# Kernel optimization log

Measured on AMD Instinct MI355X. Metric: run time of the kernel, lower is better.

Reference implementation:

```python
import jax, jax.numpy as jnp
import numpy as np

NFEAT = 128
NHID = 64
NLAYER = 3
N_NODES = 50000
N_EDGES = 800000
N_GRAPHS = 512
BN_EPS = 1e-5


def _bn(x, gamma, beta):
    # BatchNorm1d in training mode: biased batch stats over the node axis.
    m = x.mean(axis=0)
    v = x.var(axis=0)
    return (x - m) * jax.lax.rsqrt(v + BN_EPS) * gamma + beta


def _pool(x, batch):
    # global_mean_pool: segment mean over graph ids.
    s = jax.ops.segment_sum(x, batch, num_segments=N_GRAPHS)
    c = jax.ops.segment_sum(jnp.ones((x.shape[0], 1), x.dtype), batch, num_segments=N_GRAPHS)
    return s / jnp.maximum(c, 1.0)


def setup_inputs() -> dict:
    key = jax.random.key(0)
    ks = jax.random.split(key, 16)
    x = jax.random.normal(ks[0], (N_NODES, NFEAT), dtype=jnp.float32)
    edge_index = jax.random.randint(ks[1], (2, N_EDGES), 0, N_NODES, dtype=jnp.int64)
    batch = jnp.sort(jax.random.randint(ks[2], (N_NODES,), 0, N_GRAPHS, dtype=jnp.int64))
    s_in = 1.0 / np.sqrt(NFEAT)
    s_h = 1.0 / np.sqrt(NHID)
    return {
        "x": x,
        "edge_index": edge_index,
        "batch": batch,
        "Wt": jax.random.uniform(ks[3], (NFEAT, NHID), jnp.float32, -s_in, s_in),
        "bt": jax.random.uniform(ks[4], (NHID,), jnp.float32, -s_in, s_in),
        "gt": jnp.ones((NHID,), jnp.float32),
        "bet": jnp.zeros((NHID,), jnp.float32),
        "W1": jax.random.uniform(ks[5], (NLAYER, NHID, NHID), jnp.float32, -s_h, s_h),
        "b1": jax.random.uniform(ks[6], (NLAYER, NHID), jnp.float32, -s_h, s_h),
        "W2": jax.random.uniform(ks[7], (NLAYER, NHID, NHID), jnp.float32, -s_h, s_h),
        "b2": jax.random.uniform(ks[8], (NLAYER, NHID), jnp.float32, -s_h, s_h),
        "g": jnp.ones((NLAYER, NHID), jnp.float32),
        "be": jnp.zeros((NLAYER, NHID), jnp.float32),
    }


def reference(x, edge_index, batch, Wt, bt, gt, bet, W1, b1, W2, b2, g, be):
    n = x.shape[0]
    src, dst = edge_index[0], edge_index[1]
    # input transform: Linear + BN
    h = _bn(x @ Wt + bt, gt, bet)
    embeds = [_pool(h, batch)]
    for l in range(NLAYER):
        # GINConv, eps=0: mlp(x_i + sum_{j->i} x_j); flow source->target
        agg = jax.ops.segment_sum(h[src], dst, num_segments=n)
        z = h + agg
        z = jax.nn.relu(z @ W1[l] + b1[l]) @ W2[l] + b2[l]
        h = jax.nn.relu(_bn(z, g[l], be[l]))
        embeds.append(_pool(h, batch))
    return jnp.stack(embeds)  # [NLAYER+1, N_GRAPHS, NHID]
```

## Files before the change

### kernel.cpp

```cpp
#include <hip/hip_runtime.h>

#define NFEAT   128
#define NHID    64
#define NLAYER  3
#define NNODES  50000
#define NEDGES  800000
#define NGRAPHS 512
#define BN_EPS  1e-5f
#define MLPB    1563
#define CAP     64
#define PADW    68

typedef unsigned short u16;
typedef __attribute__((ext_vector_type(8))) short bf8;
typedef __attribute__((ext_vector_type(4))) float f32x4;

__device__ inline float b2f(u16 v) { return __uint_as_float(((unsigned)v) << 16); }
__device__ inline u16 f2b(float f) {
    unsigned u = __float_as_uint(f);
    return (u16)((u + 0x7FFF + ((u >> 16) & 1)) >> 16);
}
__device__ inline bf8 ldb8(const u16* p) {
    union { uint2 a[2]; bf8 v; } u;
    u.a[0] = *(const uint2*)p;
    u.a[1] = *(const uint2*)(p + 4);
    return u.v;
}
__device__ inline bf8 ldb8g(const u16* p) {
    union { uint4 a; bf8 v; } u;
    u.a = *(const uint4*)p;
    return u.v;
}
__device__ inline void add8(float* a, const uint4 v) {
    a[0] += __uint_as_float(v.x << 16);
    a[1] += __uint_as_float(v.x & 0xFFFF0000u);
    a[2] += __uint_as_float(v.y << 16);
    a[3] += __uint_as_float(v.y & 0xFFFF0000u);
    a[4] += __uint_as_float(v.z << 16);
    a[5] += __uint_as_float(v.z & 0xFFFF0000u);
    a[6] += __uint_as_float(v.w << 16);
    a[7] += __uint_as_float(v.w & 0xFFFF0000u);
}
__device__ inline void unp8(float* a, const uint4 v) {
    a[0] = __uint_as_float(v.x << 16);
    a[1] = __uint_as_float(v.x & 0xFFFF0000u);
    a[2] = __uint_as_float(v.y << 16);
    a[3] = __uint_as_float(v.y & 0xFFFF0000u);
    a[4] = __uint_as_float(v.z << 16);
    a[5] = __uint_as_float(v.z & 0xFFFF0000u);
    a[6] = __uint_as_float(v.w << 16);
    a[7] = __uint_as_float(v.w & 0xFFFF0000u);
}
__device__ inline uint2 pack4(float a, float b, float c, float d) {
    uint2 r;
    r.x = (unsigned)f2b(a) | ((unsigned)f2b(b) << 16);
    r.y = (unsigned)f2b(c) | ((unsigned)f2b(d) << 16);
    return r;
}

__global__ __launch_bounds__(256) void k_fill(const int* __restrict__ ei,
                                              int* __restrict__ deg,
                                              int* __restrict__ col) {
    int rangeId = blockIdx.x & 7, chunk = blockIdx.x >> 3;
    int lo = rangeId * (NNODES / 8), hi = lo + (NNODES / 8);
    int ebeg = chunk * (NEDGES / 256), eend = ebeg + (NEDGES / 256);
    for (int e = ebeg + threadIdx.x; e < eend; e += 256) {
        int dst = ei[NEDGES + e];
        if (dst >= lo && dst < hi) {
            int slot = atomicAdd(&deg[dst], 1);
            if (slot < CAP) col[dst * CAP + slot] = ei[e];
        }
    }
}

__global__ __launch_bounds__(256) void k_goff(const int* __restrict__ batch,
                                              int* __restrict__ gstart) {
    int gph = blockIdx.x * 256 + threadIdx.x;
    if (gph > NGRAPHS) return;
    if (gph == NGRAPHS) { gstart[NGRAPHS] = NNODES; return; }
    int lo = 0, hi = NNODES;
    while (lo < hi) {
        int mid = (lo + hi) >> 1;
        if (batch[mid] < gph) lo = mid + 1; else hi = mid;
    }
    gstart[gph] = lo;
}

__global__ __launch_bounds__(256) void k_wcvt(const float* __restrict__ Wt,
                                              const float* __restrict__ W1,
                                              const float* __restrict__ W2,
                                              u16* __restrict__ wtin,
                                              u16* __restrict__ wt) {
    int idx = blockIdx.x * 256 + threadIdx.x;
    if (idx < NFEAT * NHID) {
        int n = idx >> 7, k = idx & 127;
        wtin[n * NFEAT + k] = f2b(Wt[k * NHID + n]);
        return;
    }
    idx -= NFEAT * NHID;
    if (idx < NLAYER * NHID * NHID) {
        int l = idx >> 12, rem = idx & 4095, n = rem >> 6, k = rem & 63;
        wt[l * 8192 + n * 64 + k]        = f2b(W1[l * 4096 + k * 64 + n]);
        wt[l * 8192 + 4096 + n * 64 + k] = f2b(W2[l * 4096 + k * 64 + n]);
    }
}

__global__ __launch_bounds__(256) void k_gemm_in(const float* __restrict__ x,
                                                 const u16* __restrict__ wtin,
                                                 const float* __restrict__ bt,
                                                 u16* __restrict__ zout,
                                                 float* __restrict__ partials) {
    __shared__ u16 sx[32][132];
    __shared__ float ps[128];
    int tid = threadIdx.x;
    int base = blockIdx.x * 32;
#pragma unroll
    for (int i = 0; i < 4; ++i) {
        int idx = i * 256 + tid;
        int row = idx >> 5, kq = idx & 31;
        int rc = min(base + row, NNODES - 1);
        float4 v = ((const float4*)(x + (long long)rc * NFEAT))[kq];
        *(uint2*)&sx[row][kq * 4] = pack4(v.x, v.y, v.z, v.w);
    }
    __syncthreads();
    int w = tid >> 6, lane = tid & 63;
    int m = lane & 15, g = lane >> 4;
    int ncol = w * 16 + m;
    bool hiv = (base + 16 < NNODES);
    float bb = bt[ncol];
    f32x4 cl = {bb, bb, bb, bb}, ch = {bb, bb, bb, bb};
    const u16* wn = wtin + ncol * NFEAT;
#pragma unroll
    for (int s = 0; s < 4; ++s) {
        int k0 = s * 32 + g * 8;
        bf8 B  = ldb8g(wn + k0);
        bf8 Al = ldb8(&sx[m][k0]);
        bf8 Ah = ldb8(&sx[16 + m][k0]);
        cl = __builtin_amdgcn_mfma_f32_16x16x32_bf16(Al, B, cl, 0, 0, 0);
        ch = __builtin_amdgcn_mfma_f32_16x16x32_bf16(Ah, B, ch, 0, 0, 0);
    }
    float s1 = cl[0] + cl[1] + cl[2] + cl[3];
    float s2 = cl[0] * cl[0] + cl[1] * cl[1] + cl[2] * cl[2] + cl[3] * cl[3];
    if (hiv) {
        s1 += ch[0] + ch[1] + ch[2] + ch[3];
        s2 += ch[0] * ch[0] + ch[1] * ch[1] + ch[2] * ch[2] + ch[3] * ch[3];
    }
    s1 += __shfl_xor(s1, 16, 64); s1 += __shfl_xor(s1, 32, 64);
    s2 += __shfl_xor(s2, 16, 64); s2 += __shfl_xor(s2, 32, 64);
    if (lane < 16) {
        ps[w * 16 + lane] = s1;
        ps[64 + w * 16 + lane] = s2;
    }
#pragma unroll
    for (int i = 0; i < 4; ++i) {
        zout[(base + g * 4 + i) * NHID + ncol] = f2b(cl[i]);
        if (hiv) zout[(base + 16 + g * 4 + i) * NHID + ncol] = f2b(ch[i]);
    }
    __syncthreads();
    if (tid < 128) partials[blockIdx.x * 128 + tid] = ps[tid];
}

__global__ __launch_bounds__(256) void k_red(const float* __restrict__ partials,
                                             float* __restrict__ stats, int np) {
    __shared__ float red[4];
    int c = blockIdx.x, t = threadIdx.x;
    float s = 0.f;
    for (int i = t; i < np; i += 256) s += partials[i * 128 + c];
#pragma unroll
    for (int off = 32; off >= 1; off >>= 1) s += __shfl_xor(s, off, 64);
    if ((t & 63) == 0) red[t >> 6] = s;
    __syncthreads();
    if (t == 0) stats[c] = red[0] + red[1] + red[2] + red[3];
}

__global__ __launch_bounds__(256) void k_bnh(const u16* __restrict__ z,
                                             const float* __restrict__ stats,
                                             const float* __restrict__ gamma,
                                             const float* __restrict__ beta,
                                             u16* __restrict__ h) {
    int idx = blockIdx.x * 256 + threadIdx.x;
    if (idx >= NNODES * NHID / 8) return;
    int j0 = (idx & 7) * 8;
    uint4 v = ((const uint4*)z)[idx];
    float o[8];
    unp8(o, v);
#pragma unroll
    for (int k = 0; k < 8; ++k) {
        int j = j0 + k;
        float m = stats[j] * (1.0f / NNODES);
        float var = stats[64 + j] * (1.0f / NNODES) - m * m;
        float sc = rsqrtf(var + BN_EPS) * gamma[j];
        o[k] = fmaxf(fmaf(o[k], sc, beta[j] - m * sc), 0.f);
    }
    uint4 w;
    uint2 p0 = pack4(o[0], o[1], o[2], o[3]);
    uint2 p1 = pack4(o[4], o[5], o[6], o[7]);
    w.x = p0.x; w.y = p0.y; w.z = p1.x; w.w = p1.y;
    ((uint4*)h)[idx] = w;
}

__global__ __launch_bounds__(256) void k_pool(const u16* __restrict__ z,
                                              const float* __restrict__ stats,
                                              const float* __restrict__ gamma,
                                              const float* __restrict__ beta,
                                              const int* __restrict__ gstart,
                                              float* __restrict__ out) {
    __shared__ float4 red[4][16];
    int gph = blockIdx.x;
    int lane = threadIdx.x & 63, w = threadIdx.x >> 6;
    int c = lane & 15, ws = lane >> 4;
    int slot = w * 4 + ws;
    int j0 = c * 4;
    float sc[4], sh[4];
#pragma unroll
    for (int k = 0; k < 4; ++k) {
        int j = j0 + k;
        float m = stats[j] * (1.0f / NNODES);
        float var = stats[64 + j] * (1.0f / NNODES) - m * m;
        sc[k] = rsqrtf(var + BN_EPS) * gamma[j];
        sh[k] = beta[j] - m * sc[k];
    }
    const ushort4* z4 = (const ushort4*)z;
    int s0 = gstart[gph], e0 = gstart[gph + 1];
    float a[4] = {0.f, 0.f, 0.f, 0.f};
    for (int r = s0 + slot; r < e0; r += 16) {
        ushort4 v = z4[r * 16 + c];
        a[0] += fmaxf(fmaf(b2f(v.x), sc[0], sh[0]), 0.f);
        a[1] += fmaxf(fmaf(b2f(v.y), sc[1], sh[1]), 0.f);
        a[2] += fmaxf(fmaf(b2f(v.z), sc[2], sh[2]), 0.f);
        a[3] += fmaxf(fmaf(b2f(v.w), sc[3], sh[3]), 0.f);
    }
#pragma unroll
    for (int k = 0; k < 4; ++k) {
        a[k] += __shfl_xor(a[k], 16, 64);
        a[k] += __shfl_xor(a[k], 32, 64);
    }
    if (lane < 16) red[w][c] = make_float4(a[0], a[1], a[2], a[3]);
    __syncthreads();
    if (threadIdx.x < 16) {
        float4 r0 = red[0][threadIdx.x], r1 = red[1][threadIdx.x];
        float4 r2 = red[2][threadIdx.x], r3 = red[3][threadIdx.x];
        float inv = 1.0f / fmaxf((float)(e0 - s0), 1.0f);
        float* o = &out[gph * NHID + threadIdx.x * 4];
        o[0] = (r0.x + r1.x + r2.x + r3.x) * inv;
        o[1] = (r0.y + r1.y + r2.y + r3.y) * inv;
        o[2] = (r0.z + r1.z + r2.z + r3.z) * inv;
        o[3] = (r0.w + r1.w + r2.w + r3.w) * inv;
    }
}

template <int AFFINE>
__global__ __launch_bounds__(256) void k_mlp(const u16* __restrict__ hin,
                                             const float* __restrict__ stats,
                                             const float* __restrict__ gamma,
                                             const float* __restrict__ beta,
                                             const int* __restrict__ batch,
                                             const int* __restrict__ deg,
                                             const int* __restrict__ col,
                                             const u16* __restrict__ w1t,
                                             const float* __restrict__ b1,
                                             const u16* __restrict__ w2t,
                                             const float* __restrict__ b2,
                                             u16* __restrict__ zout,
                                             float* __restrict__ partials,
                                             float* __restrict__ poolacc) {
    __shared__ u16 szb[32][PADW];
    __shared__ u16 stb[32][PADW];
    __shared__ float ps[128];
    int tid = threadIdx.x;
    int w = tid >> 6, lane = tid & 63;
    int nd = lane >> 3, c8 = lane & 7;
    int node = w * 8 + nd;
    int base = blockIdx.x * 32;
    int r = base + node;
    bool rv = (r < NNODES);
    int rc = rv ? r : (NNODES - 1);
    const uint4* h16 = (const uint4*)hin;

    float sc[8], sh[8];
    if (AFFINE) {
#pragma unroll
        for (int k = 0; k < 8; ++k) {
            int j = c8 * 8 + k;
            float m = stats[j] * (1.0f / NNODES);
            float var = stats[64 + j] * (1.0f / NNODES) - m * m;
            sc[k] = rsqrtf(var + BN_EPS) * gamma[j];
            sh[k] = beta[j] - m * sc[k];
        }
    }

    float acc[8], acc2[8] = {0, 0, 0, 0, 0, 0, 0, 0};
    float selfh[8];
    {
        uint4 sv = h16[rc * 8 + c8];
        unp8(acc, sv);
#pragma unroll
        for (int k = 0; k < 8; ++k)
            selfh[k] = AFFINE ? fmaf(acc[k], sc[k], sh[k]) : acc[k];
    }
    int dd = rv ? min(deg[r], CAP) : 0;
    {
        const int* cp = col + rc * CAP;
        int t = 0;
        for (; t + 8 <= dd; t += 8) {
            int4 ia = *(const int4*)(cp + t);
            int4 ib = *(const int4*)(cp + t + 4);
            uint4 v0 = h16[ia.x * 8 + c8];
            uint4 v1 = h16[ia.y * 8 + c8];
            uint4 v2 = h16[ia.z * 8 + c8];
            uint4 v3 = h16[ia.w * 8 + c8];
            uint4 v4 = h16[ib.x * 8 + c8];
            uint4 v5 = h16[ib.y * 8 + c8];
            uint4 v6 = h16[ib.z * 8 + c8];
            uint4 v7 = h16[ib.w * 8 + c8];
            add8(acc, v0); add8(acc2, v1); add8(acc, v2); add8(acc2, v3);
            add8(acc, v4); add8(acc2, v5); add8(acc, v6); add8(acc2, v7);
        }
        if (t + 4 <= dd) {
            int4 ia = *(const int4*)(cp + t);
            uint4 v0 = h16[ia.x * 8 + c8];
            uint4 v1 = h16[ia.y * 8 + c8];
            uint4 v2 = h16[ia.z * 8 + c8];
            uint4 v3 = h16[ia.w * 8 + c8];
            add8(acc, v0); add8(acc2, v1); add8(acc, v2); add8(acc2, v3);
            t += 4;
        }
        for (; t < dd; ++t) {
            uint4 v0 = h16[cp[t] * 8 + c8];
            add8(acc, v0);
        }
    }
    {
        float zv[8];
#pragma unroll
        for (int k = 0; k < 8; ++k) {
            float s = acc[k] + acc2[k];
            zv[k] = AFFINE ? fmaf(s, sc[k], (float)(1 + dd) * sh[k]) : s;
            if (!rv) zv[k] = 0.f;
        }
        *(uint2*)&szb[node][c8 * 8]     = pack4(zv[0], zv[1], zv[2], zv[3]);
        *(uint2*)&szb[node][c8 * 8 + 4] = pack4(zv[4], zv[5], zv[6], zv[7]);
    }

    {
        int r0 = base + w * 8;
        int myg = rv ? batch[r] : -1;
        int g_lo = batch[min(r0, NNODES - 1)];
        int g_hi = batch[min(r0 + 7, NNODES - 1)];
        for (int gg = g_lo; gg <= g_hi; ++gg) {
            float v[8];
#pragma unroll
            for (int k = 0; k < 8; ++k) {
                v[k] = (myg == gg) ? selfh[k] : 0.f;
                v[k] += __shfl_xor(v[k], 8, 64);
                v[k] += __shfl_xor(v[k], 16, 64);
                v[k] += __shfl_xor(v[k], 32, 64);
            }
            if (lane < 8) {
                float* p = &poolacc[gg * NHID + lane * 8];
#pragma unroll
                for (int k = 0; k < 8; ++k) atomicAdd(p + k, v[k]);
            }
        }
    }
    __syncthreads();

    int m = lane & 15, g = lane >> 4;
    int ncol = w * 16 + m;
    bool hiv = (base + 16 < NNODES);
    const u16* w1n = w1t + ncol * 64;
    const u16* w2n = w2t + ncol * 64;

    bf8 Al0 = ldb8(&szb[m][g * 8]);
    bf8 Al1 = ldb8(&szb[m][32 + g * 8]);
    bf8 Ah0 = ldb8(&szb[16 + m][g * 8]);
    bf8 Ah1 = ldb8(&szb[16 + m][32 + g * 8]);
    bf8 B0 = ldb8g(w1n + g * 8);
    bf8 B1 = ldb8g(w1n + 32 + g * 8);
    float bb1 = b1[ncol];
    f32x4 cl = {bb1, bb1, bb1, bb1}, ch = {bb1, bb1, bb1, bb1};
    cl = __builtin_amdgcn_mfma_f32_16x16x32_bf16(Al0, B0, cl, 0, 0, 0);
    cl = __builtin_amdgcn_mfma_f32_16x16x32_bf16(Al1, B1, cl, 0, 0, 0);
    ch = __builtin_amdgcn_mfma_f32_16x16x32_bf16(Ah0, B0, ch, 0, 0, 0);
    ch = __builtin_amdgcn_mfma_f32_16x16x32_bf16(Ah1, B1, ch, 0, 0, 0);
#pragma unroll
    for (int i = 0; i < 4; ++i) {
        stb[g * 4 + i][ncol]      = f2b(fmaxf(cl[i], 0.f));
        stb[16 + g * 4 + i][ncol] = f2b(fmaxf(ch[i], 0.f));
    }
    __syncthreads();

    bf8 Cl0 = ldb8(&stb[m][g * 8]);
    bf8 Cl1 = ldb8(&stb[m][32 + g * 8]);
    bf8 Ch0 = ldb8(&stb[16 + m][g * 8]);
    bf8 Ch1 = ldb8(&stb[16 + m][32 + g * 8]);
    bf8 D0 = ldb8g(w2n + g * 8);
    bf8 D1 = ldb8g(w2n + 32 + g * 8);
    float bb2 = b2[ncol];
    f32x4 el = {bb2, bb2, bb2, bb2}, eh = {bb2, bb2, bb2, bb2};
    el = __builtin_amdgcn_mfma_f32_16x16x32_bf16(Cl0, D0, el, 0, 0, 0);
    el = __builtin_amdgcn_mfma_f32_16x16x32_bf16(Cl1, D1, el, 0, 0, 0);
    eh = __builtin_amdgcn_mfma_f32_16x16x32_bf16(Ch0, D0, eh, 0, 0, 0);
    eh = __builtin_amdgcn_mfma_f32_16x16x32_bf16(Ch1, D1, eh, 0, 0, 0);

    float s1 = el[0] + el[1] + el[2] + el[3];
    float s2 = el[0] * el[0] + el[1] * el[1] + el[2] * el[2] + el[3] * el[3];
    if (hiv) {
        s1 += eh[0] + eh[1] + eh[2] + eh[3];
        s2 += eh[0] * eh[0] + eh[1] * eh[1] + eh[2] * eh[2] + eh[3] * eh[3];
    }
    s1 += __shfl_xor(s1, 16, 64); s1 += __shfl_xor(s1, 32, 64);
    s2 += __shfl_xor(s2, 16, 64); s2 += __shfl_xor(s2, 32, 64);
    if (lane < 16) {
        ps[w * 16 + lane] = s1;
        ps[64 + w * 16 + lane] = s2;
    }
#pragma unroll
    for (int i = 0; i < 4; ++i) {
        zout[(base + g * 4 + i) * NHID + ncol] = f2b(el[i]);
        if (hiv) zout[(base + 16 + g * 4 + i) * NHID + ncol] = f2b(eh[i]);
    }
    __syncthreads();
    if (tid < 128) partials[blockIdx.x * 128 + tid] = ps[tid];
}

__global__ __launch_bounds__(256) void k_final(const float* __restrict__ poolacc,
                                               const int* __restrict__ gstart,
                                               float* __restrict__ out) {
    int idx = blockIdx.x * 256 + threadIdx.x;
    if (idx >= NLAYER * NGRAPHS * NHID) return;
    int g = (idx >> 6) & (NGRAPHS - 1);
    float cnt = (float)(gstart[g + 1] - gstart[g]);
    out[idx] = poolacc[idx] / fmaxf(cnt, 1.0f);
}

extern "C" void kernel_launch(void* const* d_in, const int* in_sizes, int n_in,
                              void* d_out, int out_size, void* d_ws, size_t ws_size,
                              hipStream_t stream) {
    const float* x     = (const float*)d_in[0];
    const int*   ei    = (const int*)d_in[1];
    const int*   batch = (const int*)d_in[2];
    const float* Wt    = (const float*)d_in[3];
    const float* bt    = (const float*)d_in[4];
    const float* gt    = (const float*)d_in[5];
    const float* bet   = (const float*)d_in[6];
    const float* W1    = (const float*)d_in[7];
    const float* b1    = (const float*)d_in[8];
    const float* W2    = (const float*)d_in[9];
    const float* b2    = (const float*)d_in[10];
    const float* g     = (const float*)d_in[11];
    const float* be    = (const float*)d_in[12];
    float* out = (float*)d_out;

    u16* A          = (u16*)d_ws;
    u16* B          = A + NNODES * NHID;
    u16* H          = B + NNODES * NHID;
    u16* wt         = H + NNODES * NHID;
    u16* wtin       = wt + NLAYER * 2 * NHID * NHID;
    float* partials = (float*)(wtin + NFEAT * NHID);
    float* stats    = partials + MLPB * 128;
    int* deg        = (int*)(stats + 4 * 128);
    float* poolacc  = (float*)(deg + NNODES);
    int* col        = (int*)(poolacc + NLAYER * NGRAPHS * NHID);
    int* gstart     = col + NNODES * CAP;

    hipMemsetAsync(deg, 0, (NNODES + NLAYER * NGRAPHS * NHID) * sizeof(int), stream);

    k_fill<<<2048, 256, 0, stream>>>(ei, deg, col);
    k_goff<<<3, 256, 0, stream>>>(batch, gstart);
    k_wcvt<<<80, 256, 0, stream>>>(Wt, W1, W2, wtin, wt);

    k_gemm_in<<<MLPB, 256, 0, stream>>>(x, wtin, bt, A, partials);
    k_red<<<128, 256, 0, stream>>>(partials, stats, MLPB);

    k_mlp<1><<<MLPB, 256, 0, stream>>>(A, stats, gt, bet, batch, deg, col,
                                       wt, b1, wt + 4096, b2,
                                       B, partials, poolacc);
    k_red<<<128, 256, 0, stream>>>(partials, stats + 128, MLPB);

    k_bnh<<<MLPB, 256, 0, stream>>>(B, stats + 128, g, be, H);
    k_mlp<0><<<MLPB, 256, 0, stream>>>(H, stats + 128, g, be, batch, deg, col,
                                       wt + 8192, b1 + NHID, wt + 8192 + 4096, b2 + NHID,
                                       A, partials, poolacc + NGRAPHS * NHID);
    k_red<<<128, 256, 0, stream>>>(partials, stats + 256, MLPB);

    k_bnh<<<MLPB, 256, 0, stream>>>(A, stats + 256, g + NHID, be + NHID, H);
    k_mlp<0><<<MLPB, 256, 0, stream>>>(H, stats + 256, g + NHID, be + NHID, batch, deg, col,
                                       wt + 16384, b1 + 2 * NHID, wt + 16384 + 4096, b2 + 2 * NHID,
                                       B, partials, poolacc + 2 * NGRAPHS * NHID);
    k_red<<<128, 256, 0, stream>>>(partials, stats + 384, MLPB);

    k_pool<<<NGRAPHS, 256, 0, stream>>>(B, stats + 384, g + 2 * NHID, be + 2 * NHID,
                                        gstart, out + NLAYER * NGRAPHS * NHID);
    k_final<<<(NLAYER * NGRAPHS * NHID + 255) / 256, 256, 0, stream>>>(poolacc, gstart, out);
}
```

Before: 202.5 us.

## Drop stats reduction kernels via atomics, merge setup kernels, use 16-bit neighbor indices

Each GEMM/MLP block now adds its per-column BN sum and sum-of-squares straight into the global stats with float atomics. This removes the partials buffer and all four k_red launches. The graph-offset binary search is folded into the weight-conversion kernel, which saves another launch. Neighbor column indices are stored as u16, since node ids stay below 65536, which halves the index traffic in the aggregation gather. The cost is contention on 128 atomic addresses and a nondeterministic summation order.

```diff
diff --git a/kernel.cpp b/kernel.cpp
--- a/kernel.cpp
+++ b/kernel.cpp
@@ -60,7 +60,7 @@
 
 __global__ __launch_bounds__(256) void k_fill(const int* __restrict__ ei,
                                               int* __restrict__ deg,
-                                              int* __restrict__ col) {
+                                              u16* __restrict__ col) {
     int rangeId = blockIdx.x & 7, chunk = blockIdx.x >> 3;
     int lo = rangeId * (NNODES / 8), hi = lo + (NNODES / 8);
     int ebeg = chunk * (NEDGES / 256), eend = ebeg + (NEDGES / 256);
@@ -68,29 +68,18 @@
         int dst = ei[NEDGES + e];
         if (dst >= lo && dst < hi) {
             int slot = atomicAdd(&deg[dst], 1);
-            if (slot < CAP) col[dst * CAP + slot] = ei[e];
-        }
-    }
-}
-
-__global__ __launch_bounds__(256) void k_goff(const int* __restrict__ batch,
-                                              int* __restrict__ gstart) {
-    int gph = blockIdx.x * 256 + threadIdx.x;
-    if (gph > NGRAPHS) return;
-    if (gph == NGRAPHS) { gstart[NGRAPHS] = NNODES; return; }
-    int lo = 0, hi = NNODES;
-    while (lo < hi) {
-        int mid = (lo + hi) >> 1;
-        if (batch[mid] < gph) lo = mid + 1; else hi = mid;
-    }
-    gstart[gph] = lo;
-}
-
-__global__ __launch_bounds__(256) void k_wcvt(const float* __restrict__ Wt,
-                                              const float* __restrict__ W1,
-                                              const float* __restrict__ W2,
-                                              u16* __restrict__ wtin,
-                                              u16* __restrict__ wt) {
+            if (slot < CAP) col[dst * CAP + slot] = (u16)ei[e];
+        }
+    }
+}
+
+__global__ __launch_bounds__(256) void k_setup(const float* __restrict__ Wt,
+                                               const float* __restrict__ W1,
+                                               const float* __restrict__ W2,
+                                               const int* __restrict__ batch,
+                                               u16* __restrict__ wtin,
+                                               u16* __restrict__ wt,
+                                               int* __restrict__ gstart) {
     int idx = blockIdx.x * 256 + threadIdx.x;
     if (idx < NFEAT * NHID) {
         int n = idx >> 7, k = idx & 127;
@@ -102,6 +91,17 @@
         int l = idx >> 12, rem = idx & 4095, n = rem >> 6, k = rem & 63;
         wt[l * 8192 + n * 64 + k]        = f2b(W1[l * 4096 + k * 64 + n]);
         wt[l * 8192 + 4096 + n * 64 + k] = f2b(W2[l * 4096 + k * 64 + n]);
+        return;
+    }
+    idx -= NLAYER * NHID * NHID;
+    if (idx <= NGRAPHS) {
+        if (idx == NGRAPHS) { gstart[NGRAPHS] = NNODES; return; }
+        int lo = 0, hi = NNODES;
+        while (lo < hi) {
+            int mid = (lo + hi) >> 1;
+            if (batch[mid] < idx) lo = mid + 1; else hi = mid;
+        }
+        gstart[idx] = lo;
     }
 }
 
@@ -109,9 +109,8 @@
                                                  const u16* __restrict__ wtin,
                                                  const float* __restrict__ bt,
                                                  u16* __restrict__ zout,
-                                                 float* __restrict__ partials) {
+                                                 float* __restrict__ stats) {
     __shared__ u16 sx[32][132];
-    __shared__ float ps[128];
     int tid = threadIdx.x;
     int base = blockIdx.x * 32;
 #pragma unroll
@@ -148,29 +147,14 @@
     s1 += __shfl_xor(s1, 16, 64); s1 += __shfl_xor(s1, 32, 64);
     s2 += __shfl_xor(s2, 16, 64); s2 += __shfl_xor(s2, 32, 64);
     if (lane < 16) {
-        ps[w * 16 + lane] = s1;
-        ps[64 + w * 16 + lane] = s2;
+        atomicAdd(&stats[w * 16 + lane], s1);
+        atomicAdd(&stats[64 + w * 16 + lane], s2);
     }
 #pragma unroll
     for (int i = 0; i < 4; ++i) {
         zout[(base + g * 4 + i) * NHID + ncol] = f2b(cl[i]);
         if (hiv) zout[(base + 16 + g * 4 + i) * NHID + ncol] = f2b(ch[i]);
     }
-    __syncthreads();
-    if (tid < 128) partials[blockIdx.x * 128 + tid] = ps[tid];
-}
-
-__global__ __launch_bounds__(256) void k_red(const float* __restrict__ partials,
-                                             float* __restrict__ stats, int np) {
-    __shared__ float red[4];
-    int c = blockIdx.x, t = threadIdx.x;
-    float s = 0.f;
-    for (int i = t; i < np; i += 256) s += partials[i * 128 + c];
-#pragma unroll
-    for (int off = 32; off >= 1; off >>= 1) s += __shfl_xor(s, off, 64);
-    if ((t & 63) == 0) red[t >> 6] = s;
-    __syncthreads();
-    if (t == 0) stats[c] = red[0] + red[1] + red[2] + red[3];
 }
 
 __global__ __launch_bounds__(256) void k_bnh(const u16* __restrict__ z,
@@ -256,17 +240,16 @@
                                              const float* __restrict__ beta,
                                              const int* __restrict__ batch,
                                              const int* __restrict__ deg,
-                                             const int* __restrict__ col,
+                                             const u16* __restrict__ col,
                                              const u16* __restrict__ w1t,
                                              const float* __restrict__ b1,
                                              const u16* __restrict__ w2t,
                                              const float* __restrict__ b2,
                                              u16* __restrict__ zout,
-                                             float* __restrict__ partials,
+                                             float* __restrict__ statsout,
                                              float* __restrict__ poolacc) {
     __shared__ u16 szb[32][PADW];
     __shared__ u16 stb[32][PADW];
-    __shared__ float ps[128];
     int tid = threadIdx.x;
     int w = tid >> 6, lane = tid & 63;
     int nd = lane >> 3, c8 = lane & 7;
@@ -300,33 +283,38 @@
     }
     int dd = rv ? min(deg[r], CAP) : 0;
     {
-        const int* cp = col + rc * CAP;
+        const u16* cp = col + rc * CAP;
         int t = 0;
         for (; t + 8 <= dd; t += 8) {
-            int4 ia = *(const int4*)(cp + t);
-            int4 ib = *(const int4*)(cp + t + 4);
-            uint4 v0 = h16[ia.x * 8 + c8];
-            uint4 v1 = h16[ia.y * 8 + c8];
-            uint4 v2 = h16[ia.z * 8 + c8];
-            uint4 v3 = h16[ia.w * 8 + c8];
-            uint4 v4 = h16[ib.x * 8 + c8];
-            uint4 v5 = h16[ib.y * 8 + c8];
-            uint4 v6 = h16[ib.z * 8 + c8];
-            uint4 v7 = h16[ib.w * 8 + c8];
+            uint4 iv = *(const uint4*)(cp + t);
+            int s0 = iv.x & 0xFFFF, s1 = iv.x >> 16;
+            int s2 = iv.y & 0xFFFF, s3 = iv.y >> 16;
+            int s4 = iv.z & 0xFFFF, s5 = iv.z >> 16;
+            int s6 = iv.w & 0xFFFF, s7 = iv.w >> 16;
+            uint4 v0 = h16[s0 * 8 + c8];
+            uint4 v1 = h16[s1 * 8 + c8];
+            uint4 v2 = h16[s2 * 8 + c8];
+            uint4 v3 = h16[s3 * 8 + c8];
+            uint4 v4 = h16[s4 * 8 + c8];
+            uint4 v5 = h16[s5 * 8 + c8];
+            uint4 v6 = h16[s6 * 8 + c8];
+            uint4 v7 = h16[s7 * 8 + c8];
             add8(acc, v0); add8(acc2, v1); add8(acc, v2); add8(acc2, v3);
             add8(acc, v4); add8(acc2, v5); add8(acc, v6); add8(acc2, v7);
         }
         if (t + 4 <= dd) {
-            int4 ia = *(const int4*)(cp + t);
-            uint4 v0 = h16[ia.x * 8 + c8];
-            uint4 v1 = h16[ia.y * 8 + c8];
-            uint4 v2 = h16[ia.z * 8 + c8];
-            uint4 v3 = h16[ia.w * 8 + c8];
+            uint2 iv = *(const uint2*)(cp + t);
+            int s0 = iv.x & 0xFFFF, s1 = iv.x >> 16;
+            int s2 = iv.y & 0xFFFF, s3 = iv.y >> 16;
+            uint4 v0 = h16[s0 * 8 + c8];
+            uint4 v1 = h16[s1 * 8 + c8];
+            uint4 v2 = h16[s2 * 8 + c8];
+            uint4 v3 = h16[s3 * 8 + c8];
             add8(acc, v0); add8(acc2, v1); add8(acc, v2); add8(acc2, v3);
             t += 4;
         }
         for (; t < dd; ++t) {
-            uint4 v0 = h16[cp[t] * 8 + c8];
+            uint4 v0 = h16[(int)cp[t] * 8 + c8];
             add8(acc, v0);
         }
     }
@@ -412,16 +400,14 @@
     s1 += __shfl_xor(s1, 16, 64); s1 += __shfl_xor(s1, 32, 64);
     s2 += __shfl_xor(s2, 16, 64); s2 += __shfl_xor(s2, 32, 64);
     if (lane < 16) {
-        ps[w * 16 + lane] = s1;
-        ps[64 + w * 16 + lane] = s2;
+        atomicAdd(&statsout[w * 16 + lane], s1);
+        atomicAdd(&statsout[64 + w * 16 + lane], s2);
     }
 #pragma unroll
     for (int i = 0; i < 4; ++i) {
         zout[(base + g * 4 + i) * NHID + ncol] = f2b(el[i]);
         if (hiv) zout[(base + 16 + g * 4 + i) * NHID + ncol] = f2b(eh[i]);
     }
-    __syncthreads();
-    if (tid < 128) partials[blockIdx.x * 128 + tid] = ps[tid];
 }
 
 __global__ __launch_bounds__(256) void k_final(const float* __restrict__ poolacc,
@@ -457,38 +443,33 @@
     u16* H          = B + NNODES * NHID;
     u16* wt         = H + NNODES * NHID;
     u16* wtin       = wt + NLAYER * 2 * NHID * NHID;
-    float* partials = (float*)(wtin + NFEAT * NHID);
-    float* stats    = partials + MLPB * 128;
-    int* deg        = (int*)(stats + 4 * 128);
+    int* deg        = (int*)(wtin + NFEAT * NHID);
     float* poolacc  = (float*)(deg + NNODES);
-    int* col        = (int*)(poolacc + NLAYER * NGRAPHS * NHID);
-    int* gstart     = col + NNODES * CAP;
-
-    hipMemsetAsync(deg, 0, (NNODES + NLAYER * NGRAPHS * NHID) * sizeof(int), stream);
+    float* stats    = poolacc + NLAYER * NGRAPHS * NHID;
+    u16* col        = (u16*)(stats + 4 * 128);
+    int* gstart     = (int*)(col + NNODES * CAP);
+
+    size_t zbytes = NNODES * sizeof(int) + (NLAYER * NGRAPHS * NHID + 4 * 128) * sizeof(float);
+    hipMemsetAsync(deg, 0, zbytes, stream);
 
     k_fill<<<2048, 256, 0, stream>>>(ei, deg, col);
-    k_goff<<<3, 256, 0, stream>>>(batch, gstart);
-    k_wcvt<<<80, 256, 0, stream>>>(Wt, W1, W2, wtin, wt);
-
-    k_gemm_in<<<MLPB, 256, 0, stream>>>(x, wtin, bt, A, partials);
-    k_red<<<128, 256, 0, stream>>>(partials, stats, MLPB);
+    k_setup<<<83, 256, 0, stream>>>(Wt, W1, W2, batch, wtin, wt, gstart);
+
+    k_gemm_in<<<MLPB, 256, 0, stream>>>(x, wtin, bt, A, stats);
 
     k_mlp<1><<<MLPB, 256, 0, stream>>>(A, stats, gt, bet, batch, deg, col,
                                        wt, b1, wt + 4096, b2,
-                                       B, partials, poolacc);
-    k_red<<<128, 256, 0, stream>>>(partials, stats + 128, MLPB);
+                                       B, stats + 128, poolacc);
 
     k_bnh<<<MLPB, 256, 0, stream>>>(B, stats + 128, g, be, H);
     k_mlp<0><<<MLPB, 256, 0, stream>>>(H, stats + 128, g, be, batch, deg, col,
                                        wt + 8192, b1 + NHID, wt + 8192 + 4096, b2 + NHID,
-                                       A, partials, poolacc + NGRAPHS * NHID);
-    k_red<<<128, 256, 0, stream>>>(partials, stats + 256, MLPB);
+                                       A, stats + 256, poolacc + NGRAPHS * NHID);
 
     k_bnh<<<MLPB, 256, 0, stream>>>(A, stats + 256, g + NHID, be + NHID, H);
     k_mlp<0><<<MLPB, 256, 0, stream>>>(H, stats + 256, g + NHID, be + NHID, batch, deg, col,
                                        wt + 16384, b1 + 2 * NHID, wt + 16384 + 4096, b2 + 2 * NHID,
-                                       B, partials, poolacc + 2 * NGRAPHS * NHID);
-    k_red<<<128, 256, 0, stream>>>(partials, stats + 384, MLPB);
+                                       B, stats + 384, poolacc + 2 * NGRAPHS * NHID);
 
     k_pool<<<NGRAPHS, 256, 0, stream>>>(B, stats + 384, g + 2 * NHID, be + 2 * NHID,
                                         gstart, out + NLAYER * NGRAPHS * NHID);
```

Result: slower. 319.3 us (+57.7%).
